# Optimization experiments

Measured on AMD Instinct MI355X. Metric: run time of the kernel, lower is better.

Reference implementation:

```python
import jax, jax.numpy as jnp
import numpy as np

L, N, E = 2048, 8, 1024
H = 16
KP = 256
KSZ = L // KP  # conv kernel size and stride = 8


def setup_inputs() -> dict:
    key = jax.random.key(0)
    ks = jax.random.split(key, 10)
    s = 0.02
    return {
        "query": jax.random.normal(ks[0], (L, N, E), jnp.float32),
        "key": jax.random.normal(ks[1], (L, N, E), jnp.float32),
        "value": jax.random.normal(ks[2], (L, N, E), jnp.float32),
        "in_proj_w": jax.random.normal(ks[3], (3 * E, E), jnp.float32) * s,
        "in_proj_b": jnp.zeros((3 * E,), jnp.float32),
        "e_w": jax.random.normal(ks[4], (E, E, KSZ), jnp.float32) * s,  # Conv1d OIH
        "e_b": jnp.zeros((E,), jnp.float32),
        "f_w": jax.random.normal(ks[5], (E, E, KSZ), jnp.float32) * s,
        "f_b": jnp.zeros((E,), jnp.float32),
        "out_w": jax.random.normal(ks[6], (E, E), jnp.float32) * s,
        "out_b": jnp.zeros((E,), jnp.float32),
    }


def _compress(x, w, b):
    # x: (S, N, E) -> conv1d over seq with kernel=stride=KSZ -> (Kp, N, E)
    xc = jnp.transpose(x, (1, 2, 0))  # (N, E, S)
    y = jax.lax.conv_general_dilated(
        xc, w, window_strides=(KSZ,), padding="VALID",
        dimension_numbers=("NCH", "OIH", "NCH"))
    y = y + b[None, :, None]
    return jnp.transpose(y, (2, 0, 1))  # (Kp, N, E)


def reference(query, key, value, in_proj_w, in_proj_b, e_w, e_b, f_w, f_b, out_w, out_b):
    D = E // H
    scaling = D ** -0.5
    q = query @ in_proj_w[:E].T + in_proj_b[:E]
    k = key @ in_proj_w[E:2 * E].T + in_proj_b[E:2 * E]
    v = value @ in_proj_w[2 * E:].T + in_proj_b[2 * E:]
    q = q * scaling
    k = _compress(k, e_w, e_b)  # (Kp, N, E)
    v = _compress(v, f_w, f_b)
    Kp = k.shape[0]
    # reshape to (N*H, len, D)
    qh = jnp.transpose(q.reshape(L, N * H, D), (1, 0, 2))
    kh = jnp.transpose(k.reshape(Kp, N * H, D), (1, 0, 2))
    vh = jnp.transpose(v.reshape(Kp, N * H, D), (1, 0, 2))
    attn = jax.nn.softmax(jnp.einsum("bld,bkd->blk", qh, kh), axis=-1)
    out = jnp.einsum("blk,bkd->bld", attn, vh)  # (N*H, L, D)
    out = jnp.transpose(out, (1, 0, 2)).reshape(L, N, E)
    out = out @ out_w.T + out_b
    attn_weights = attn.reshape(N, H, L, Kp).mean(axis=1)  # need_weights avg over heads
    return out, attn_weights
```

## Files before the change

### kernel.cpp

```cpp
#include <hip/hip_runtime.h>

typedef unsigned short u16;
typedef u16  u16x4 __attribute__((ext_vector_type(4)));
typedef u16  u16x8 __attribute__((ext_vector_type(8)));
typedef float f32x4 __attribute__((ext_vector_type(4)));
typedef int   i32x4 __attribute__((ext_vector_type(4)));
typedef __bf16 bf16x8 __attribute__((ext_vector_type(8)));

#define LSEQ 2048
#define NB 8
#define EDIM 1024
#define HNUM 16
#define DDIM 64
#define KPDIM 256
#define NE (NB*EDIM)
#define MROWS (LSEQ*NB)
#define AWSZ ((size_t)NB*LSEQ*KPDIM)

__device__ __forceinline__ u16 f2b(float f) {
  unsigned u = __builtin_bit_cast(unsigned, f);
  u += 0x7fffu + ((u >> 16) & 1u);
  return (u16)(u >> 16);
}

__device__ __forceinline__ void gl_lds16(const void* g, void* l) {
  __builtin_amdgcn_global_load_lds(
      (const __attribute__((address_space(1))) void*)g,
      (__attribute__((address_space(3))) void*)l, 16, 0, 0);
}

__device__ __forceinline__ f32x4 mfma16(bf16x8 a, bf16x8 b, f32x4 c) {
  return __builtin_amdgcn_mfma_f32_16x16x32_bf16(a, b, c, 0, 0, 0);
}

#define BAR()   __builtin_amdgcn_s_barrier()
#define LGKM0() asm volatile("s_waitcnt lgkmcnt(0)" ::: "memory")
#define WVM6()  asm volatile("s_waitcnt vmcnt(6)" ::: "memory")
#define WVM0()  asm volatile("s_waitcnt vmcnt(0)" ::: "memory")

__global__ void prep1(const float* __restrict__ ipw, const float* __restrict__ ow,
                      const float* __restrict__ ipb, u16* __restrict__ w_in,
                      u16* __restrict__ w_out, float* __restrict__ bq) {
  int i = blockIdx.x * blockDim.x + threadIdx.x;
  if (i < 786432) {
    f32x4 v = ((const f32x4*)ipw)[i];
    float s = (i < 262144) ? 0.125f : 1.0f;
    u16x4 o;
    o[0] = f2b(v[0] * s); o[1] = f2b(v[1] * s);
    o[2] = f2b(v[2] * s); o[3] = f2b(v[3] * s);
    ((u16x4*)w_in)[i] = o;
  }
  if (i < 262144) {
    f32x4 v = ((const f32x4*)ow)[i];
    u16x4 o;
    o[0] = f2b(v[0]); o[1] = f2b(v[1]); o[2] = f2b(v[2]); o[3] = f2b(v[3]);
    ((u16x4*)w_out)[i] = o;
  }
  if (i < 256) {
    f32x4 b = ((const f32x4*)ipb)[i];
    ((f32x4*)bq)[i] = b * 0.125f;
  }
}

__global__ void wtrans(const float* __restrict__ ew, const float* __restrict__ fw,
                       u16* __restrict__ eT, u16* __restrict__ fT) {
  const float* src = blockIdx.y ? fw : ew;
  u16* dst = blockIdx.y ? fT : eT;
  int eo = blockIdx.x >> 4;
  int ei0 = (blockIdx.x & 15) * 64;
  int l = threadIdx.x;
  __shared__ u16 lds[8][64];
  const float* s = src + (size_t)eo * 8192 + (size_t)ei0 * 8 + l * 8;
  f32x4 a = *(const f32x4*)s;
  f32x4 b = *(const f32x4*)(s + 4);
  float v[8] = {a[0], a[1], a[2], a[3], b[0], b[1], b[2], b[3]};
#pragma unroll
  for (int t = 0; t < 8; ++t) lds[t][l] = f2b(v[t]);
  __syncthreads();
  int t = l >> 3, c = l & 7;
  i32x4 out = *(const i32x4*)&lds[t][c * 8];
  *(i32x4*)(dst + (size_t)eo * 8192 + t * 1024 + ei0 + c * 8) = out;
}

__global__ void castqkv(const float* __restrict__ q, const float* __restrict__ k,
                        const float* __restrict__ v, u16* __restrict__ out) {
  const float* src = blockIdx.y == 0 ? q : (blockIdx.y == 1 ? k : v);
  size_t base = (size_t)blockIdx.y * ((size_t)MROWS * EDIM);
  size_t i = ((size_t)blockIdx.x * 256 + threadIdx.x) * 8;
  f32x4 v0 = *(const f32x4*)(src + i);
  f32x4 v1 = *(const f32x4*)(src + i + 4);
  u16x8 o;
  o[0] = f2b(v0[0]); o[1] = f2b(v0[1]); o[2] = f2b(v0[2]); o[3] = f2b(v0[3]);
  o[4] = f2b(v1[0]); o[5] = f2b(v1[1]); o[6] = f2b(v1[2]); o[7] = f2b(v1[3]);
  *(u16x8*)(out + base + i) = o;
}

__global__ void redc(const float* __restrict__ part, const float* __restrict__ eb,
                     const float* __restrict__ fb, u16* __restrict__ kc,
                     u16* __restrict__ vcT) {
  int zc = blockIdx.y;
  const float* p = part + (size_t)zc * 4 * 2048 * 1024;
  const float* bias = zc ? fb : eb;
  size_t i = ((size_t)blockIdx.x * 256 + threadIdx.x) * 4;
  f32x4 s = *(const f32x4*)(p + i);
  s += *(const f32x4*)(p + 2097152 + i);
  s += *(const f32x4*)(p + 2 * 2097152 + i);
  s += *(const f32x4*)(p + 3 * 2097152 + i);
  int e = (int)(i & 1023);
  int row = (int)(i >> 10);
  int n = row >> 8, pp = row & 255;
  int h = e >> 6, d = e & 63;
  f32x4 b = *(const f32x4*)(bias + e);
  if (zc == 0) {
    u16x4 o;
    o[0] = f2b(s[0] + b[0]); o[1] = f2b(s[1] + b[1]);
    o[2] = f2b(s[2] + b[2]); o[3] = f2b(s[3] + b[3]);
    *(u16x4*)(kc + (((size_t)(n * HNUM + h) * KPDIM + pp) * DDIM + d)) = o;
  } else {
    size_t base = (size_t)(n * HNUM + h) * (DDIM * KPDIM);
#pragma unroll
    for (int q = 0; q < 4; ++q) {
      int dq = d + q;
      vcT[base + dq * 256 + (((pp >> 3) ^ (dq & 7)) * 8) + (pp & 7)] =
          f2b(s[q] + b[q]);
    }
  }
}

__global__ void awred(const float* __restrict__ awp, float* __restrict__ aw) {
  size_t i = ((size_t)blockIdx.x * 256 + threadIdx.x) * 4;
  f32x4 s = *(const f32x4*)(awp + i);
  s += *(const f32x4*)(awp + AWSZ + i);
  s += *(const f32x4*)(awp + 2 * AWSZ + i);
  s += *(const f32x4*)(awp + 3 * AWSZ + i);
  *(f32x4*)(aw + i) = s;
}

template<int AMODE, int OUTMODE>
__global__ __launch_bounds__(512, 2)
void gemm256(const void* A0p, const void* A1p, const void* A2p,
             const u16* B0p, const u16* B1p, const u16* B2p,
             const float* b0p, const float* b1p, const float* b2p,
             void* C0p, void* C1p, void* C2p,
             int M, int K, int kspl) {
  const int zc = blockIdx.z / kspl, sp = blockIdx.z % kspl;
  const void* Ap = zc == 0 ? A0p : (zc == 1 ? A1p : A2p);
  const u16* Bp = zc == 0 ? B0p : (zc == 1 ? B1p : B2p);
  const float* biasp = zc == 0 ? b0p : (zc == 1 ? b1p : b2p);
  void* Cp = zc == 0 ? C0p : (zc == 1 ? C1p : C2p);

  __shared__ u16 lds[2][2][2][128 * 64];

  const int tid = threadIdx.x;
  const int w = tid >> 6, lane = tid & 63;
  const int lr = lane & 15, lg = lane >> 4;
  const int wr = w >> 2, wc = w & 3;
  const int m0 = blockIdx.x * 256, n0 = blockIdx.y * 256;
  const int kper = K / kspl, kbase = sp * kper, nt = kper >> 6;

  f32x4 acc[8][4];
#pragma unroll
  for (int mi = 0; mi < 8; ++mi)
#pragma unroll
    for (int ni = 0; ni < 4; ++ni) {
      f32x4 zv = {0.f, 0.f, 0.f, 0.f};
      acc[mi][ni] = zv;
    }

  auto stage_half = [&](int buf, int op, int half, int kt) {
    const int k0 = kbase + (kt << 6);
#pragma unroll
    for (int i = 0; i < 2; ++i) {
      int c = i * 512 + tid;
      int r = c >> 3, j = c & 7, js = j ^ (r & 7);
      int row = half * 128 + r;
      u16* dst = &lds[buf][op][half][c * 8];
      if (op == 1) {
        gl_lds16(Bp + (size_t)(n0 + row) * K + k0 + js * 8, dst);
      } else if (AMODE == 0) {
        gl_lds16((const u16*)Ap + (size_t)(m0 + row) * K + k0 + js * 8, dst);
      } else {
        int m = m0 + row;
        int nn = m >> 8, p = m & 255;
        int k = k0 + js * 8;
        gl_lds16((const u16*)Ap + (size_t)(p * 8 + (k >> 10)) * NE +
                 nn * EDIM + (k & 1023), dst);
      }
    }
  };

  auto LDA = [&](int buf, int row, int ks) -> bf16x8 {
    return *(const bf16x8*)&lds[buf][0][row >> 7]
        [(row & 127) * 64 + (((ks * 4 + lg) ^ (row & 7)) << 3)];
  };
  auto LDB = [&](int buf, int row, int ks) -> bf16x8 {
    return *(const bf16x8*)&lds[buf][1][row >> 7]
        [(row & 127) * 64 + (((ks * 4 + lg) ^ (row & 7)) << 3)];
  };

  stage_half(0, 0, 0, 0); stage_half(0, 1, 0, 0);
  stage_half(0, 1, 1, 0); stage_half(0, 0, 1, 0);
  if (nt > 1) {
    stage_half(1, 1, 0, 1); stage_half(1, 1, 1, 1); stage_half(1, 0, 0, 1);
    WVM6();
  } else {
    WVM0();
  }
  BAR();

  for (int t = 0; t < nt; t += 2) {
    bf16x8 a0[4][2], a1[4][2], b0f[2][2], b1f[2][2];
#pragma unroll
    for (int mi = 0; mi < 4; ++mi)
#pragma unroll
      for (int ks = 0; ks < 2; ++ks)
        a0[mi][ks] = LDA(0, wr * 128 + mi * 16 + lr, ks);
#pragma unroll
    for (int ni = 0; ni < 2; ++ni)
#pragma unroll
      for (int ks = 0; ks < 2; ++ks)
        b0f[ni][ks] = LDB(0, wc * 64 + ni * 16 + lr, ks);
    stage_half(1, 0, 1, t + 1);
    BAR(); LGKM0();
    __builtin_amdgcn_s_setprio(1);
#pragma unroll
    for (int mi = 0; mi < 4; ++mi)
#pragma unroll
      for (int ni = 0; ni < 2; ++ni)
#pragma unroll
        for (int ks = 0; ks < 2; ++ks)
          acc[mi][ni] = mfma16(a0[mi][ks], b0f[ni][ks], acc[mi][ni]);
    __builtin_amdgcn_s_setprio(0);
    BAR();
#pragma unroll
    for (int ni = 0; ni < 2; ++ni)
#pragma unroll
      for (int ks = 0; ks < 2; ++ks)
        b1f[ni][ks] = LDB(0, wc * 64 + (ni + 2) * 16 + lr, ks);
    BAR(); LGKM0();
    __builtin_amdgcn_s_setprio(1);
#pragma unroll
    for (int mi = 0; mi < 4; ++mi)
#pragma unroll
      for (int ni = 0; ni < 2; ++ni)
#pragma unroll
        for (int ks = 0; ks < 2; ++ks)
          acc[mi][ni + 2] = mfma16(a0[mi][ks], b1f[ni][ks], acc[mi][ni + 2]);
    __builtin_amdgcn_s_setprio(0);
    BAR();
#pragma unroll
    for (int mi = 0; mi < 4; ++mi)
#pragma unroll
      for (int ks = 0; ks < 2; ++ks)
        a1[mi][ks] = LDA(0, wr * 128 + 64 + mi * 16 + lr, ks);
    if (t + 2 < nt) stage_half(0, 1, 0, t + 2);
    BAR(); LGKM0();
    __builtin_amdgcn_s_setprio(1);
#pragma unroll
    for (int mi = 0; mi < 4; ++mi)
#pragma unroll
      for (int ni = 0; ni < 2; ++ni)
#pragma unroll
        for (int ks = 0; ks < 2; ++ks)
          acc[mi + 4][ni + 2] = mfma16(a1[mi][ks], b1f[ni][ks], acc[mi + 4][ni + 2]);
    __builtin_amdgcn_s_setprio(0);
    BAR();
    if (t + 2 < nt) { stage_half(0, 1, 1, t + 2); stage_half(0, 0, 0, t + 2); }
    BAR();
    __builtin_amdgcn_s_setprio(1);
#pragma unroll
    for (int mi = 0; mi < 4; ++mi)
#pragma unroll
      for (int ni = 0; ni < 2; ++ni)
#pragma unroll
        for (int ks = 0; ks < 2; ++ks)
          acc[mi + 4][ni] = mfma16(a1[mi][ks], b0f[ni][ks], acc[mi + 4][ni]);
    __builtin_amdgcn_s_setprio(0);
    if (t + 2 < nt) { WVM6(); } else { WVM0(); }
    BAR();
#pragma unroll
    for (int mi = 0; mi < 4; ++mi)
#pragma unroll
      for (int ks = 0; ks < 2; ++ks)
        a0[mi][ks] = LDA(1, wr * 128 + mi * 16 + lr, ks);
#pragma unroll
    for (int ni = 0; ni < 2; ++ni)
#pragma unroll
      for (int ks = 0; ks < 2; ++ks)
        b0f[ni][ks] = LDB(1, wc * 64 + ni * 16 + lr, ks);
    if (t + 2 < nt) stage_half(0, 0, 1, t + 2);
    BAR(); LGKM0();
    __builtin_amdgcn_s_setprio(1);
#pragma unroll
    for (int mi = 0; mi < 4; ++mi)
#pragma unroll
      for (int ni = 0; ni < 2; ++ni)
#pragma unroll
        for (int ks = 0; ks < 2; ++ks)
          acc[mi][ni] = mfma16(a0[mi][ks], b0f[ni][ks], acc[mi][ni]);
    __builtin_amdgcn_s_setprio(0);
    BAR();
#pragma unroll
    for (int ni = 0; ni < 2; ++ni)
#pragma unroll
      for (int ks = 0; ks < 2; ++ks)
        b1f[ni][ks] = LDB(1, wc * 64 + (ni + 2) * 16 + lr, ks);
    BAR(); LGKM0();
    __builtin_amdgcn_s_setprio(1);
#pragma unroll
    for (int mi = 0; mi < 4; ++mi)
#pragma unroll
      for (int ni = 0; ni < 2; ++ni)
#pragma unroll
        for (int ks = 0; ks < 2; ++ks)
          acc[mi][ni + 2] = mfma16(a0[mi][ks], b1f[ni][ks], acc[mi][ni + 2]);
    __builtin_amdgcn_s_setprio(0);
    BAR();
#pragma unroll
    for (int mi = 0; mi < 4; ++mi)
#pragma unroll
      for (int ks = 0; ks < 2; ++ks)
        a1[mi][ks] = LDA(1, wr * 128 + 64 + mi * 16 + lr, ks);
    if (t + 3 < nt) stage_half(1, 1, 0, t + 3);
    BAR(); LGKM0();
    __builtin_amdgcn_s_setprio(1);
#pragma unroll
    for (int mi = 0; mi < 4; ++mi)
#pragma unroll
      for (int ni = 0; ni < 2; ++ni)
#pragma unroll
        for (int ks = 0; ks < 2; ++ks)
          acc[mi + 4][ni + 2] = mfma16(a1[mi][ks], b1f[ni][ks], acc[mi + 4][ni + 2]);
    __builtin_amdgcn_s_setprio(0);
    BAR();
    if (t + 3 < nt) { stage_half(1, 1, 1, t + 3); stage_half(1, 0, 0, t + 3); }
    BAR();
    __builtin_amdgcn_s_setprio(1);
#pragma unroll
    for (int mi = 0; mi < 4; ++mi)
#pragma unroll
      for (int ni = 0; ni < 2; ++ni)
#pragma unroll
        for (int ks = 0; ks < 2; ++ks)
          acc[mi + 4][ni] = mfma16(a1[mi][ks], b0f[ni][ks], acc[mi + 4][ni]);
    __builtin_amdgcn_s_setprio(0);
    if (t + 3 < nt) { WVM6(); } else { WVM0(); }
    BAR();
  }

  if (OUTMODE == 0) {
    __syncthreads();
    u16* cw = (u16*)&lds[0][0][0][0];
#pragma unroll
    for (int ni = 0; ni < 4; ++ni) {
      const int col = wc * 64 + ni * 16 + lr;
      const float bv = biasp[n0 + col];
#pragma unroll
      for (int mi = 0; mi < 8; ++mi)
#pragma unroll
        for (int j = 0; j < 4; ++j) {
          const int row = wr * 128 + mi * 16 + lg * 4 + j;
          cw[row * 256 + col] = f2b(acc[mi][ni][j] + bv);
        }
    }
    __syncthreads();
#pragma unroll
    for (int it = 0; it < 16; ++it) {
      int c = it * 512 + tid;
      int row = c >> 5, ch = c & 31;
      i32x4 v = *(const i32x4*)&cw[row * 256 + ch * 8];
      *(i32x4*)((u16*)Cp + (size_t)(m0 + row) * 1024 + n0 + ch * 8) = v;
    }
  } else {
#pragma unroll
    for (int ni = 0; ni < 4; ++ni) {
      const int col = n0 + wc * 64 + ni * 16 + lr;
      const float bv = (OUTMODE == 2) ? 0.f : biasp[col];
#pragma unroll
      for (int mi = 0; mi < 8; ++mi)
#pragma unroll
        for (int j = 0; j < 4; ++j) {
          const int row = m0 + wr * 128 + mi * 16 + lg * 4 + j;
          const float v = acc[mi][ni][j] + bv;
          if (OUTMODE == 2)
            ((float*)Cp)[(size_t)sp * M * 1024 + (size_t)row * 1024 + col] = v;
          else
            ((float*)Cp)[(size_t)row * 1024 + col] = v;
        }
    }
  }
}

template<int AMODE, int OUTMODE>
__global__ __launch_bounds__(256)
void gemm_bt(const void* A0p, const void* A1p, const void* A2p,
             const u16* B0p, const u16* B1p, const u16* B2p,
             const float* b0p, const float* b1p, const float* b2p,
             void* C0p, void* C1p, void* C2p,
             int M, int K, int kspl) {
  const int zc = blockIdx.z / kspl;
  const int sp = blockIdx.z % kspl;
  const void* Ap = zc == 0 ? A0p : (zc == 1 ? A1p : A2p);
  const u16* Bp = zc == 0 ? B0p : (zc == 1 ? B1p : B2p);
  const float* biasp = zc == 0 ? b0p : (zc == 1 ? b1p : b2p);
  void* Cp = zc == 0 ? C0p : (zc == 1 ? C1p : C2p);

  __shared__ u16 Alds[128 * 64];
  __shared__ u16 Blds[128 * 64];

  const int tid = threadIdx.x;
  const int w = tid >> 6, lane = tid & 63;
  const int lr = lane & 15, lg = lane >> 4;
  const int m0 = blockIdx.x * 128, n0 = blockIdx.y * 128;
  const int wr = (w >> 1) * 64, wc = (w & 1) * 64;
  const int brow = lane >> 3;
  const int bcol = (lane & 7) * 8;

  f32x4 acc[4][4];
#pragma unroll
  for (int mi = 0; mi < 4; ++mi)
#pragma unroll
    for (int ni = 0; ni < 4; ++ni) {
      f32x4 zv = {0.f, 0.f, 0.f, 0.f};
      acc[mi][ni] = zv;
    }

  const int kper = K / kspl;
  const int ktn = kper >> 6;
  const int kb = sp * kper;
  for (int kt = 0; kt < ktn; ++kt) {
    const int k0 = kb + (kt << 6);
    __syncthreads();
#pragma unroll
    for (int i = 0; i < 4; ++i) {
      const int c = w * 4 + i;
      const int row = c * 8 + brow;
      gl_lds16(Bp + (size_t)(n0 + row) * K + k0 + bcol, &Blds[c * 512]);
    }
    if (AMODE == 2) {
      const float* Af = (const float*)Ap;
#pragma unroll
      for (int i = 0; i < 4; ++i) {
        const int c = i * 256 + tid;
        const int row = c >> 3, k8 = (c & 7) * 8;
        const float* s = Af + (size_t)(m0 + row) * K + k0 + k8;
        f32x4 v0 = *(const f32x4*)s;
        f32x4 v1 = *(const f32x4*)(s + 4);
        u16x8 pk;
        pk[0] = f2b(v0[0]); pk[1] = f2b(v0[1]); pk[2] = f2b(v0[2]); pk[3] = f2b(v0[3]);
        pk[4] = f2b(v1[0]); pk[5] = f2b(v1[1]); pk[6] = f2b(v1[2]); pk[7] = f2b(v1[3]);
        *(u16x8*)&Alds[row * 64 + k8] = pk;
      }
    } else if (AMODE == 0) {
      const u16* Ab = (const u16*)Ap;
#pragma unroll
      for (int i = 0; i < 4; ++i) {
        const int c = w * 4 + i;
        const int row = c * 8 + brow;
        gl_lds16(Ab + (size_t)(m0 + row) * K + k0 + bcol, &Alds[c * 512]);
      }
    } else {
      const u16* Ab = (const u16*)Ap;
#pragma unroll
      for (int i = 0; i < 4; ++i) {
        const int c = w * 4 + i;
        const int m = m0 + c * 8 + brow;
        const int nn = m >> 8, p = m & 255;
        const int k = k0 + bcol;
        gl_lds16(Ab + (size_t)(p * 8 + (k >> 10)) * NE + nn * EDIM + (k & 1023),
                 &Alds[c * 512]);
      }
    }
    __syncthreads();
#pragma unroll
    for (int ks = 0; ks < 2; ++ks) {
      bf16x8 af[4], bf[4];
#pragma unroll
      for (int mi = 0; mi < 4; ++mi)
        af[mi] = *(const bf16x8*)&Alds[(wr + mi * 16 + lr) * 64 + ks * 32 + lg * 8];
#pragma unroll
      for (int ni = 0; ni < 4; ++ni)
        bf[ni] = *(const bf16x8*)&Blds[(wc + ni * 16 + lr) * 64 + ks * 32 + lg * 8];
#pragma unroll
      for (int mi = 0; mi < 4; ++mi)
#pragma unroll
        for (int ni = 0; ni < 4; ++ni)
          acc[mi][ni] = mfma16(af[mi], bf[ni], acc[mi][ni]);
    }
  }
#pragma unroll
  for (int ni = 0; ni < 4; ++ni) {
    const int col = n0 + wc + ni * 16 + lr;
    const float bv = (OUTMODE == 2) ? 0.f : biasp[col];
#pragma unroll
    for (int mi = 0; mi < 4; ++mi)
#pragma unroll
      for (int j = 0; j < 4; ++j) {
        const int row = m0 + wr + mi * 16 + lg * 4 + j;
        const float v = acc[mi][ni][j] + bv;
        if (OUTMODE == 4) {
          const int nn = row >> 8, pp = row & 255, h = col >> 6, d = col & 63;
          ((u16*)Cp)[(size_t)(nn * HNUM + h) * (DDIM * KPDIM) + d * 256 +
                     (((pp >> 3) ^ (d & 7)) * 8) + (pp & 7)] = f2b(v);
        } else if (OUTMODE == 3) {
          const int nn = row >> 8, pp = row & 255, h = col >> 6, d = col & 63;
          ((u16*)Cp)[((size_t)(nn * HNUM + h) * KPDIM + pp) * DDIM + d] = f2b(v);
        } else if (OUTMODE == 2)
          ((float*)Cp)[(size_t)sp * M * 1024 + (size_t)row * 1024 + col] = v;
        else if (OUTMODE == 1)
          ((float*)Cp)[(size_t)row * 1024 + col] = v;
        else
          ((u16*)Cp)[(size_t)row * 1024 + col] = f2b(v);
      }
  }
}

__global__ __launch_bounds__(256)
void attn_fused(const u16* __restrict__ Q, const u16* __restrict__ Kc,
                const u16* __restrict__ VcT, u16* __restrict__ Aout,
                float* __restrict__ AWp, int hpg) {
  __shared__ u16 Ares[256 * 64];
  __shared__ u16 Bres[64 * 256];
  const int tid = threadIdx.x;
  const int w = tid >> 6, lane = tid & 63;
  const int lr = lane & 15, lg = lane >> 4;
  const int n = blockIdx.y;
  const int l0 = blockIdx.x * 64;
  const int lrow = l0 + w * 16 + lr;
  char* kbase = (char*)Ares;
  char* vbase = (char*)Bres;
  char* pbase = (char*)Ares + w * 8192;

  f32x4 macc[16];
#pragma unroll
  for (int ni = 0; ni < 16; ++ni) { f32x4 zv = {0.f,0.f,0.f,0.f}; macc[ni] = zv; }

  for (int hh = 0; hh < hpg; ++hh) {
    const int h = blockIdx.z * hpg + hh;
    const u16* kh = Kc + (size_t)(n * HNUM + h) * (KPDIM * DDIM);
    const u16* vh = VcT + (size_t)(n * HNUM + h) * (DDIM * KPDIM);
    __syncthreads();
#pragma unroll
    for (int it = 0; it < 8; ++it) {
      int c = it * 256 + tid;
      int p = c >> 3, j = c & 7;
      gl_lds16(kh + p * 64 + ((j ^ (p & 7)) << 3), kbase + c * 16);
    }
#pragma unroll
    for (int it = 0; it < 8; ++it) {
      int c = it * 256 + tid;
      gl_lds16(vh + c * 8, vbase + c * 16);
    }
    const u16* qp = Q + (size_t)lrow * NE + n * EDIM + h * DDIM + lg * 8;
    bf16x8 aq0 = *(const bf16x8*)qp;
    bf16x8 aq1 = *(const bf16x8*)(qp + 32);
    __syncthreads();
    f32x4 s[16];
#pragma unroll
    for (int ni = 0; ni < 16; ++ni) { f32x4 zv = {0.f,0.f,0.f,0.f}; s[ni] = zv; }
#pragma unroll
    for (int ni = 0; ni < 16; ++ni) {
      int row = ni * 16 + lr;
      const char* kr = kbase + row * 128;
      bf16x8 b0 = *(const bf16x8*)(kr + ((lg ^ (row & 7)) << 4));
      bf16x8 b1 = *(const bf16x8*)(kr + (((4 + lg) ^ (row & 7)) << 4));
      s[ni] = mfma16(aq0, b0, s[ni]);
      s[ni] = mfma16(aq1, b1, s[ni]);
    }
    float mx[4], sm[4], inv[4], invs[4];
#pragma unroll
    for (int j = 0; j < 4; ++j) mx[j] = -1e30f;
#pragma unroll
    for (int ni = 0; ni < 16; ++ni)
#pragma unroll
      for (int j = 0; j < 4; ++j) mx[j] = fmaxf(mx[j], s[ni][j]);
#pragma unroll
    for (int msk = 1; msk <= 8; msk <<= 1)
#pragma unroll
      for (int j = 0; j < 4; ++j) mx[j] = fmaxf(mx[j], __shfl_xor(mx[j], msk, 64));
#pragma unroll
    for (int j = 0; j < 4; ++j) sm[j] = 0.f;
#pragma unroll
    for (int ni = 0; ni < 16; ++ni)
#pragma unroll
      for (int j = 0; j < 4; ++j) {
        float e = __expf(s[ni][j] - mx[j]);
        s[ni][j] = e; sm[j] += e;
      }
#pragma unroll
    for (int msk = 1; msk <= 8; msk <<= 1)
#pragma unroll
      for (int j = 0; j < 4; ++j) sm[j] += __shfl_xor(sm[j], msk, 64);
#pragma unroll
    for (int j = 0; j < 4; ++j) { inv[j] = 1.0f / sm[j]; invs[j] = inv[j] * 0.0625f; }
    __syncthreads();
#pragma unroll
    for (int ni = 0; ni < 16; ++ni)
#pragma unroll
      for (int j = 0; j < 4; ++j) {
        macc[ni][j] += s[ni][j] * invs[j];
        int r = lg * 4 + j;
        *(u16*)(pbase + r * 512 + ((ni * 32 + lr * 2) ^ ((r & 7) << 4))) =
            f2b(s[ni][j]);
      }
    f32x4 o[4];
#pragma unroll
    for (int ni2 = 0; ni2 < 4; ++ni2) { f32x4 zv = {0.f,0.f,0.f,0.f}; o[ni2] = zv; }
#pragma unroll
    for (int ks = 0; ks < 8; ++ks) {
      bf16x8 a = *(const bf16x8*)(pbase + lr * 512 + ((ks * 64 + 16 * lg) ^ ((lr & 7) << 4)));
#pragma unroll
      for (int ni2 = 0; ni2 < 4; ++ni2) {
        int d = ni2 * 16 + lr;
        bf16x8 b = *(const bf16x8*)(vbase + d * 512 + (((ks * 4 + lg) ^ (d & 7)) << 4));
        o[ni2] = mfma16(a, b, o[ni2]);
      }
    }
#pragma unroll
    for (int ni2 = 0; ni2 < 4; ++ni2)
#pragma unroll
      for (int j = 0; j < 4; ++j) {
        int gl = l0 + w * 16 + lg * 4 + j;
        Aout[(size_t)gl * NE + n * EDIM + h * DDIM + ni2 * 16 + lr] =
            f2b(o[ni2][j] * inv[j]);
      }
  }
  float* awo = AWp + (size_t)blockIdx.z * AWSZ + (size_t)n * (LSEQ * KPDIM);
#pragma unroll
  for (int ni = 0; ni < 16; ++ni)
#pragma unroll
    for (int j = 0; j < 4; ++j) {
      int r = lg * 4 + j;
      awo[(size_t)(l0 + w * 16 + r) * KPDIM + ni * 16 + lr] = macc[ni][j];
    }
}

extern "C" void kernel_launch(void* const* d_in, const int* in_sizes, int n_in,
                              void* d_out, int out_size, void* d_ws, size_t ws_size,
                              hipStream_t stream) {
  const float* query = (const float*)d_in[0];
  const float* key   = (const float*)d_in[1];
  const float* value = (const float*)d_in[2];
  const float* ipw   = (const float*)d_in[3];
  const float* ipb   = (const float*)d_in[4];
  const float* ew    = (const float*)d_in[5];
  const float* eb    = (const float*)d_in[6];
  const float* fw    = (const float*)d_in[7];
  const float* fb    = (const float*)d_in[8];
  const float* ow    = (const float*)d_in[9];
  const float* ob    = (const float*)d_in[10];

  char* ws = (char*)d_ws;
  size_t off = 0;
  auto alloc = [&](size_t bytes) {
    void* p = ws + off;
    off += (bytes + 255) & ~(size_t)255;
    return p;
  };
  u16* qp    = (u16*)alloc((size_t)MROWS * EDIM * 2);
  u16* kp    = (u16*)alloc((size_t)MROWS * EDIM * 2);
  u16* vp    = (u16*)alloc((size_t)MROWS * EDIM * 2);
  u16* ao    = (u16*)alloc((size_t)MROWS * EDIM * 2);
  u16* kc    = (u16*)alloc((size_t)NB * KPDIM * EDIM * 2);
  u16* vcT   = (u16*)alloc((size_t)NB * KPDIM * EDIM * 2);
  u16* w_in  = (u16*)alloc((size_t)3 * EDIM * EDIM * 2);
  u16* w_eT  = (u16*)alloc((size_t)EDIM * 8 * EDIM * 2);
  u16* w_fT  = (u16*)alloc((size_t)EDIM * 8 * EDIM * 2);
  u16* w_out = (u16*)alloc((size_t)EDIM * EDIM * 2);
  float* bq  = (float*)alloc(EDIM * 4);
  size_t base_needed = off;

  size_t qkv16_b = (size_t)3 * MROWS * EDIM * 2;
  size_t part_b  = (size_t)2 * 4 * 2048 * 1024 * 4;
  bool bigX  = ws_size >= base_needed + qkv16_b;
  bool midX  = ws_size >= base_needed + part_b;
  char* X = (char*)alloc(bigX ? qkv16_b : (midX ? part_b : 0));
  u16* qkv16 = (u16*)X;
  float* part = (float*)X;
  float* awp  = (float*)X;

  float* out_f = (float*)d_out;
  float* aw_f  = (float*)d_out + (size_t)MROWS * EDIM;

  prep1<<<dim3(3072), 256, 0, stream>>>(ipw, ow, ipb, w_in, w_out, bq);
  wtrans<<<dim3(16384, 2), 64, 0, stream>>>(ew, fw, w_eT, w_fT);

  if (bigX) {
    castqkv<<<dim3(8192, 3), 256, 0, stream>>>(query, key, value, qkv16);
    gemm256<0, 0><<<dim3(64, 4, 3), 512, 0, stream>>>(
        qkv16, qkv16 + (size_t)MROWS * EDIM, qkv16 + (size_t)2 * MROWS * EDIM,
        w_in, w_in + 1048576, w_in + 2097152,
        bq, ipb + 1024, ipb + 2048,
        qp, kp, vp, MROWS, 1024, 1);
  } else {
    gemm_bt<2, 0><<<dim3(128, 8, 3), 256, 0, stream>>>(
        query, key, value,
        w_in, w_in + 1048576, w_in + 2097152,
        bq, ipb + 1024, ipb + 2048,
        qp, kp, vp, MROWS, 1024, 1);
  }

  if (bigX || midX) {
    gemm256<1, 2><<<dim3(8, 4, 8), 512, 0, stream>>>(
        kp, vp, vp,
        w_eT, w_fT, w_fT,
        eb, fb, fb,
        part, part + (size_t)4 * 2048 * 1024, part,
        NB * KPDIM, 8192, 4);
    redc<<<dim3(2048, 2), 256, 0, stream>>>(part, eb, fb, kc, vcT);
  } else {
    gemm_bt<1, 3><<<dim3(16, 8, 1), 256, 0, stream>>>(
        kp, kp, kp, w_eT, w_eT, w_eT, eb, eb, eb,
        kc, kc, kc, NB * KPDIM, 8192, 1);
    gemm_bt<1, 4><<<dim3(16, 8, 1), 256, 0, stream>>>(
        vp, vp, vp, w_fT, w_fT, w_fT, fb, fb, fb,
        vcT, vcT, vcT, NB * KPDIM, 8192, 1);
  }

  if (bigX) {
    attn_fused<<<dim3(32, 8, 4), 256, 0, stream>>>(qp, kc, vcT, ao, awp, 4);
    awred<<<dim3(4096), 256, 0, stream>>>(awp, aw_f);
  } else {
    attn_fused<<<dim3(32, 8, 1), 256, 0, stream>>>(qp, kc, vcT, ao, aw_f, 16);
  }

  gemm256<0, 1><<<dim3(64, 4, 1), 512, 0, stream>>>(
      ao, ao, ao,
      w_out, w_out, w_out,
      ob, ob, ob,
      out_f, out_f, out_f, MROWS, 1024, 1);
}
```

Before: 439.8 us.

## Keep softmax probabilities in registers via lane shuffles instead of LDS round-trip

Adds a new attention kernel that computes S^T = K·Q^T so each lane holds scores for one query row. The probabilities are packed to bf16 and redistributed with cross-lane shuffles into the MFMA A-operand layout, instead of being written to and read back from shared memory. It also prefetches the next head's K and V into LDS as soon as the current stage is done with each buffer. This removes the LDS traffic and barriers for P and overlaps loads with compute, at the cost of many shuffle instructions and higher register pressure. Only the multi-head-group (bigX) path is switched to the new kernel.

```diff
diff --git a/kernel.cpp b/kernel.cpp
--- a/kernel.cpp
+++ b/kernel.cpp
@@ -21,6 +21,10 @@
   unsigned u = __builtin_bit_cast(unsigned, f);
   u += 0x7fffu + ((u >> 16) & 1u);
   return (u16)(u >> 16);
+}
+
+__device__ __forceinline__ unsigned pk2(float a, float b) {
+  return (unsigned)f2b(a) | ((unsigned)f2b(b) << 16);
 }
 
 __device__ __forceinline__ void gl_lds16(const void* g, void* l) {
@@ -516,6 +520,141 @@
 }
 
 __global__ __launch_bounds__(256)
+void attn_fused5(const u16* __restrict__ Q, const u16* __restrict__ Kc,
+                 const u16* __restrict__ VcT, u16* __restrict__ Aout,
+                 float* __restrict__ AWp, int hpg) {
+  __shared__ u16 Kl[256 * 64];
+  __shared__ u16 Vl[64 * 256];
+  const int tid = threadIdx.x;
+  const int w = tid >> 6, lane = tid & 63;
+  const int lr = lane & 15, lg = lane >> 4;
+  const int n = blockIdx.y;
+  const int l0 = blockIdx.x * 64;
+  const int lrow = l0 + w * 16 + lr;
+  char* kbase = (char*)Kl;
+  char* vbase = (char*)Vl;
+  const int sA = lr + ((lg & 1) << 5);
+  const int sB = sA + 16;
+  const int part = lg >> 1;
+
+  auto stageK = [&](int h) {
+    const u16* kh = Kc + (size_t)(n * HNUM + h) * (KPDIM * DDIM);
+#pragma unroll
+    for (int it = 0; it < 8; ++it) {
+      int c = it * 256 + tid, p = c >> 3, j = c & 7;
+      gl_lds16(kh + p * 64 + ((j ^ (p & 7)) << 3), kbase + c * 16);
+    }
+  };
+  auto stageV = [&](int h) {
+    const u16* vh = VcT + (size_t)(n * HNUM + h) * (DDIM * KPDIM);
+#pragma unroll
+    for (int it = 0; it < 8; ++it) {
+      int c = it * 256 + tid;
+      gl_lds16(vh + c * 8, vbase + c * 16);
+    }
+  };
+
+  f32x4 macc[16];
+#pragma unroll
+  for (int ni = 0; ni < 16; ++ni) { f32x4 zv = {0.f,0.f,0.f,0.f}; macc[ni] = zv; }
+
+  const int hbase = blockIdx.z * hpg;
+  stageK(hbase); stageV(hbase);
+
+  for (int hh = 0; hh < hpg; ++hh) {
+    const int h = hbase + hh;
+    __syncthreads();
+    const u16* qp = Q + (size_t)lrow * NE + n * EDIM + h * DDIM + lg * 8;
+    bf16x8 aq0 = *(const bf16x8*)qp;
+    bf16x8 aq1 = *(const bf16x8*)(qp + 32);
+    f32x4 s[16];
+#pragma unroll
+    for (int ni = 0; ni < 16; ++ni) { f32x4 zv = {0.f,0.f,0.f,0.f}; s[ni] = zv; }
+#pragma unroll
+    for (int ni = 0; ni < 16; ++ni) {
+      int row = ni * 16 + lr;
+      const char* kr = kbase + row * 128;
+      bf16x8 k0 = *(const bf16x8*)(kr + ((lg ^ (row & 7)) << 4));
+      bf16x8 k1 = *(const bf16x8*)(kr + (((4 + lg) ^ (row & 7)) << 4));
+      s[ni] = mfma16(k0, aq0, s[ni]);
+      s[ni] = mfma16(k1, aq1, s[ni]);
+    }
+    LGKM0();
+    BAR();
+    if (hh + 1 < hpg) stageK(h + 1);
+    float mx = -1e30f;
+#pragma unroll
+    for (int ni = 0; ni < 16; ++ni)
+#pragma unroll
+      for (int j = 0; j < 4; ++j) mx = fmaxf(mx, s[ni][j]);
+    mx = fmaxf(mx, __shfl_xor(mx, 16, 64));
+    mx = fmaxf(mx, __shfl_xor(mx, 32, 64));
+    float sm = 0.f;
+#pragma unroll
+    for (int ni = 0; ni < 16; ++ni)
+#pragma unroll
+      for (int j = 0; j < 4; ++j) {
+        float e = __expf(s[ni][j] - mx);
+        s[ni][j] = e; sm += e;
+      }
+    sm += __shfl_xor(sm, 16, 64);
+    sm += __shfl_xor(sm, 32, 64);
+    const float inv = 1.0f / sm;
+#pragma unroll
+    for (int ni = 0; ni < 16; ++ni) {
+#pragma unroll
+      for (int j = 0; j < 4; ++j) s[ni][j] *= inv;
+      macc[ni] += s[ni] * 0.0625f;
+    }
+    f32x4 o[4];
+#pragma unroll
+    for (int ni2 = 0; ni2 < 4; ++ni2) { f32x4 zv = {0.f,0.f,0.f,0.f}; o[ni2] = zv; }
+#pragma unroll
+    for (int ks = 0; ks < 8; ++ks) {
+      unsigned lo0 = pk2(s[2 * ks][0], s[2 * ks][1]);
+      unsigned lo1 = pk2(s[2 * ks][2], s[2 * ks][3]);
+      unsigned hi0 = pk2(s[2 * ks + 1][0], s[2 * ks + 1][1]);
+      unsigned hi1 = pk2(s[2 * ks + 1][2], s[2 * ks + 1][3]);
+      unsigned aL0 = (unsigned)__shfl((int)lo0, sA, 64);
+      unsigned aL1 = (unsigned)__shfl((int)lo1, sA, 64);
+      unsigned aH0 = (unsigned)__shfl((int)hi0, sA, 64);
+      unsigned aH1 = (unsigned)__shfl((int)hi1, sA, 64);
+      unsigned bL0 = (unsigned)__shfl((int)lo0, sB, 64);
+      unsigned bL1 = (unsigned)__shfl((int)lo1, sB, 64);
+      unsigned bH0 = (unsigned)__shfl((int)hi0, sB, 64);
+      unsigned bH1 = (unsigned)__shfl((int)hi1, sB, 64);
+      i32x4 pu;
+      pu[0] = (int)(part ? aH0 : aL0);
+      pu[1] = (int)(part ? aH1 : aL1);
+      pu[2] = (int)(part ? bH0 : bL0);
+      pu[3] = (int)(part ? bH1 : bL1);
+      bf16x8 pa = __builtin_bit_cast(bf16x8, pu);
+#pragma unroll
+      for (int ni2 = 0; ni2 < 4; ++ni2) {
+        int d = ni2 * 16 + lr;
+        bf16x8 vf = *(const bf16x8*)(vbase + d * 512 + (((ks * 4 + lg) ^ (d & 7)) << 4));
+        o[ni2] = mfma16(pa, vf, o[ni2]);
+      }
+    }
+#pragma unroll
+    for (int ni2 = 0; ni2 < 4; ++ni2)
+#pragma unroll
+      for (int j = 0; j < 4; ++j) {
+        int gl = l0 + w * 16 + lg * 4 + j;
+        Aout[(size_t)gl * NE + n * EDIM + h * DDIM + ni2 * 16 + lr] = f2b(o[ni2][j]);
+      }
+    LGKM0();
+    BAR();
+    if (hh + 1 < hpg) stageV(h + 1);
+  }
+  float* awo = AWp + (size_t)blockIdx.z * AWSZ + (size_t)n * (LSEQ * KPDIM)
+             + (size_t)lrow * KPDIM;
+#pragma unroll
+  for (int ni = 0; ni < 16; ++ni)
+    *(f32x4*)(awo + ni * 16 + lg * 4) = macc[ni];
+}
+
+__global__ __launch_bounds__(256)
 void attn_fused(const u16* __restrict__ Q, const u16* __restrict__ Kc,
                 const u16* __restrict__ VcT, u16* __restrict__ Aout,
                 float* __restrict__ AWp, int hpg) {
@@ -718,7 +857,7 @@
   }
 
   if (bigX) {
-    attn_fused<<<dim3(32, 8, 4), 256, 0, stream>>>(qp, kc, vcT, ao, awp, 4);
+    attn_fused5<<<dim3(32, 8, 4), 256, 0, stream>>>(qp, kc, vcT, ao, awp, 4);
     awred<<<dim3(4096), 256, 0, stream>>>(awp, aw_f);
   } else {
     attn_fused<<<dim3(32, 8, 1), 256, 0, stream>>>(qp, kc, vcT, ao, aw_f, 16);
```

Measured after the change: 428.2 us. -2.6%, faster.
